# Kernel optimization log

Hardware: AMD Instinct MI355X
Metric: run time of the kernel (lower is better)

The kernel has to match this reference:

```python
import math
import jax, jax.numpy as jnp
import numpy as np

D = 1536      # d_model
H = 12        # n_heads
L = 12        # n_layers
V = 50257     # vocab (hardcoded in module)
P = 1024      # max positions (hardcoded)
B = 1         # batch (must be 1: pos-embed uses arange(len(idx)))
S = 1024      # sequence length


def setup_inputs() -> dict:
    key = jax.random.key(0)
    ks = jax.random.split(key, 10)
    sc = 0.02
    n = lambda k, shape: (jax.random.normal(k, shape, jnp.float32) * sc)
    return {
        "idx": jax.random.randint(ks[0], (B, S), 0, V),
        "mask": jnp.tril(jnp.ones((S, S), jnp.int32)),  # causal mask
        "tok_emb": n(ks[1], (V, D)),
        "pos_emb": n(ks[2], (P, D)),
        "Wqkv": n(ks[3], (L, D, 3 * D)), "bqkv": jnp.zeros((L, 3 * D), jnp.float32),
        "Wo":   n(ks[4], (L, D, D)),     "bo":   jnp.zeros((L, D), jnp.float32),
        "W1":   n(ks[5], (L, D, 4 * D)), "b1":   jnp.zeros((L, 4 * D), jnp.float32),
        "W2":   n(ks[6], (L, 4 * D, D)), "b2":   jnp.zeros((L, D), jnp.float32),
        "ln_g": jnp.ones((D,), jnp.float32), "ln_b": jnp.zeros((D,), jnp.float32),
        "Wout": n(ks[7], (D, D)), "bout": jnp.zeros((D,), jnp.float32),
    }


def _gpt_forward(idx, mask, tok_emb, pos_emb, Wqkv, bqkv, Wo, bo,
                 W1, b1, W2, b2, ln_g, ln_b, Wout, bout):
    b, s = idx.shape
    d = tok_emb.shape[1]
    hd = d // H
    scale = 1.0 / math.sqrt(d)  # note: module divides by sqrt(d_model), not head_dim

    # faithful quirk: position_embedding(arange(len(idx))) -> (B, D), broadcasts since B==1
    x = tok_emb[idx] + pos_emb[:b]  # (B,S,D)

    mask0 = (mask == 0)  # (S,S) -> broadcast over (B,H,S,S)

    def block(x, p):
        wqkv, bqkv_, wo, bo_, w1, b1_, w2, b2_ = p
        qkv = x @ wqkv + bqkv_                       # (B,S,3D)
        q, k, v = jnp.split(qkv, 3, axis=-1)
        q = q.reshape(b, s, H, hd)
        k = k.reshape(b, s, H, hd)
        v = v.reshape(b, s, H, hd)
        scores = jnp.einsum('bqhd,bkhd->bhqk', q, k) * scale
        scores = jnp.where(mask0, -jnp.inf, scores)
        attn = jax.nn.softmax(scores, axis=-2)       # non-standard: softmax over QUERY axis
        o = jnp.einsum('bhqk,bkhd->bqhd', attn, v).reshape(b, s, d)
        x = x + (o @ wo + bo_)                       # attention residual
        x = x + (jax.nn.relu(x @ w1 + b1_) @ w2 + b2_)  # FFN residual (on post-attn x)
        return x, None

    x, _ = jax.lax.scan(block, x, (Wqkv, bqkv, Wo, bo, W1, b1, W2, b2))

    # final LayerNorm (eps=1e-5 like torch default)
    mu = jnp.mean(x, axis=-1, keepdims=True)
    var = jnp.mean(jnp.square(x - mu), axis=-1, keepdims=True)
    xn = (x - mu) * jax.lax.rsqrt(var + 1e-5) * ln_g + ln_b
    return xn @ Wout + bout


def reference(idx, mask, tok_emb, pos_emb, Wqkv, bqkv, Wo, bo,
              W1, b1, W2, b2, ln_g, ln_b, Wout, bout):
    return _gpt_forward(idx, mask, tok_emb, pos_emb, Wqkv, bqkv, Wo, bo,
                        W1, b1, W2, b2, ln_g, ln_b, Wout, bout)
```

## Files before the change

kernel.cpp:

```cpp
#include <hip/hip_runtime.h>
#include <stdint.h>
#include <math.h>

#define D_MODEL 1536
#define NH 12
#define HD 128
#define NL 12
#define SEQ 1024
#define D3 4608
#define D4 6144
#define SCALE 0.025515518153991442f

typedef __attribute__((ext_vector_type(8))) short short8;
typedef __attribute__((ext_vector_type(4))) float floatx4;

__device__ __forceinline__ uint32_t packhi(float a, float b) {
  return (__float_as_uint(a) >> 16) | (__float_as_uint(b) & 0xFFFF0000u);
}
__device__ __forceinline__ float truncf32(float a) {
  return __uint_as_float(__float_as_uint(a) & 0xFFFF0000u);
}
__device__ __forceinline__ void split8v(float4 v0, float4 v1, uint4 &hi, uint4 &lo) {
  hi.x = packhi(v0.x, v0.y); hi.y = packhi(v0.z, v0.w);
  hi.z = packhi(v1.x, v1.y); hi.w = packhi(v1.z, v1.w);
  lo.x = packhi(v0.x - truncf32(v0.x), v0.y - truncf32(v0.y));
  lo.y = packhi(v0.z - truncf32(v0.z), v0.w - truncf32(v0.w));
  lo.z = packhi(v1.x - truncf32(v1.x), v1.y - truncf32(v1.y));
  lo.w = packhi(v1.z - truncf32(v1.z), v1.w - truncf32(v1.w));
}

__device__ __forceinline__ int xcd_chunk_id(int nwg) {
  int orig = blockIdx.x;
  int xcd = orig & 7, pos = orig >> 3;
  int q = nwg >> 3, r = nwg & 7;
  return (xcd < r ? xcd * (q + 1) : r * (q + 1) + (xcd - r) * q) + pos;
}

__global__ __launch_bounds__(256)
void embed_kernel(const int* __restrict__ idx, const float* __restrict__ tok,
                  const float* __restrict__ pos, float* __restrict__ x) {
  int i = blockIdx.x * 256 + threadIdx.x;
  int s = i / D_MODEL;
  int d = i - s * D_MODEL;
  x[i] = tok[(size_t)idx[s] * D_MODEL + d] + pos[d];
}

template<bool RELU, bool RES, int SPLITK, bool TA2>
__global__ __launch_bounds__(256)
void mgemm_kernel(const float* __restrict__ A, const float* __restrict__ Ab,
                  const float* __restrict__ B,
                  const float* __restrict__ bias, const float* __restrict__ res,
                  float* __restrict__ C, int M, int N, int K, int NC, int NR) {
  __shared__ short Ah[128][36], Al[128][36];
  __shared__ short Bh[64][36], Bl[64][36];
  const int tid = threadIdx.x;
  const int lane = tid & 63, wave = tid >> 6;

  const int lid = xcd_chunk_id(NC * NR * SPLITK);
  const int z   = lid / (NC * NR);
  const int rem = lid - z * (NC * NR);
  const int ct  = rem / NR;
  const int rt  = rem - ct * NR;
  const int bm = rt << 7, bn = ct << 6;

  const int wm = (wave >> 1) << 6, wn = (wave & 1) << 5;
  const int fr = lane & 15, fk = (lane >> 4) << 3;
  const int Kc = K / SPLITK;
  const int kbase = (SPLITK > 1) ? z * Kc : 0;

  floatx4 acc[4][2];
#pragma unroll
  for (int i = 0; i < 4; i++)
#pragma unroll
    for (int j = 0; j < 2; j++) acc[i][j] = (floatx4){0.f, 0.f, 0.f, 0.f};

  const int ar = tid >> 1;
  const int ac = (tid & 1) << 4;
  const int bc = tid & 63;
  const int bkq = (tid >> 6) << 3;
  const float* Ag  = A + (size_t)(bm + ar) * K + kbase + ac;
  const float* Ag2 = TA2 ? (Ab + (size_t)(bm + ar) * K + kbase + ac) : nullptr;
  const float* Bg = B + (size_t)(kbase + bkq) * N + bn + bc;

  float a_reg[16];
  float b_reg[8];

  for (int k0 = 0; k0 < Kc; k0 += 32) {
#pragma unroll
    for (int e = 0; e < 4; e++) {
      float4 v = *(const float4*)(Ag + k0 + 4 * e);
      if constexpr (TA2) {
        float4 w = *(const float4*)(Ag2 + k0 + 4 * e);
        v.x += w.x; v.y += w.y; v.z += w.z; v.w += w.w;
      }
      a_reg[4 * e + 0] = v.x; a_reg[4 * e + 1] = v.y;
      a_reg[4 * e + 2] = v.z; a_reg[4 * e + 3] = v.w;
    }
    {
      const float* Bp = Bg + (size_t)k0 * N;
#pragma unroll
      for (int j = 0; j < 8; j++) b_reg[j] = Bp[(size_t)j * N];
    }
    __syncthreads();
#pragma unroll
    for (int e = 0; e < 2; e++) {
      float4 v0 = {a_reg[8 * e + 0], a_reg[8 * e + 1], a_reg[8 * e + 2], a_reg[8 * e + 3]};
      float4 v1 = {a_reg[8 * e + 4], a_reg[8 * e + 5], a_reg[8 * e + 6], a_reg[8 * e + 7]};
      uint4 hi, lo; split8v(v0, v1, hi, lo);
      *(uint4*)&Ah[ar][ac + 8 * e] = hi;
      *(uint4*)&Al[ar][ac + 8 * e] = lo;
    }
    {
      float4 u0 = {b_reg[0], b_reg[1], b_reg[2], b_reg[3]};
      float4 u1 = {b_reg[4], b_reg[5], b_reg[6], b_reg[7]};
      uint4 hi, lo; split8v(u0, u1, hi, lo);
      *(uint4*)&Bh[bc][bkq] = hi;
      *(uint4*)&Bl[bc][bkq] = lo;
    }
    __syncthreads();

    short8 ah[4], al[4], bh[2], bl[2];
#pragma unroll
    for (int i = 0; i < 4; i++) {
      ah[i] = *(const short8*)&Ah[wm + (i << 4) + fr][fk];
      al[i] = *(const short8*)&Al[wm + (i << 4) + fr][fk];
    }
#pragma unroll
    for (int j = 0; j < 2; j++) {
      bh[j] = *(const short8*)&Bh[wn + (j << 4) + fr][fk];
      bl[j] = *(const short8*)&Bl[wn + (j << 4) + fr][fk];
    }
#pragma unroll
    for (int i = 0; i < 4; i++)
#pragma unroll
      for (int j = 0; j < 2; j++) {
        acc[i][j] = __builtin_amdgcn_mfma_f32_16x16x32_bf16(ah[i], bh[j], acc[i][j], 0, 0, 0);
        acc[i][j] = __builtin_amdgcn_mfma_f32_16x16x32_bf16(ah[i], bl[j], acc[i][j], 0, 0, 0);
        acc[i][j] = __builtin_amdgcn_mfma_f32_16x16x32_bf16(al[i], bh[j], acc[i][j], 0, 0, 0);
      }
  }

  const int cr = (lane >> 4) << 2, cc = lane & 15;
  if constexpr (SPLITK > 1) {
    float* Cp = C + (size_t)z * M * N;
#pragma unroll
    for (int j = 0; j < 2; j++) {
      const int col = bn + wn + (j << 4) + cc;
#pragma unroll
      for (int i = 0; i < 4; i++) {
        const int row0 = bm + wm + (i << 4) + cr;
#pragma unroll
        for (int r = 0; r < 4; r++)
          Cp[(size_t)(row0 + r) * N + col] = acc[i][j][r];
      }
    }
  } else {
#pragma unroll
    for (int j = 0; j < 2; j++) {
      const int col = bn + wn + (j << 4) + cc;
      const float bv = bias[col];
#pragma unroll
      for (int i = 0; i < 4; i++) {
        const int row0 = bm + wm + (i << 4) + cr;
#pragma unroll
        for (int r = 0; r < 4; r++) {
          float v = acc[i][j][r] + bv;
          if constexpr (RES) v += res[(size_t)(row0 + r) * N + col];
          if constexpr (RELU) v = fmaxf(v, 0.f);
          C[(size_t)(row0 + r) * N + col] = v;
        }
      }
    }
  }
}

template<int NP, bool HASB, bool RES, bool RELU>
__global__ __launch_bounds__(256)
void combineN_kernel(const float* __restrict__ parts, size_t pstride,
                     const float* __restrict__ bias, const float* __restrict__ res,
                     float* __restrict__ C, int N) {
  const int i = (blockIdx.x * 256 + threadIdx.x) << 2;
  float4 r = *(const float4*)&parts[i];
#pragma unroll
  for (int zz = 1; zz < NP; zz++) {
    float4 a = *(const float4*)&parts[(size_t)zz * pstride + i];
    r.x += a.x; r.y += a.y; r.z += a.z; r.w += a.w;
  }
  if constexpr (HASB) {
    const int col = i % N;
    float4 bv = *(const float4*)&bias[col];
    r.x += bv.x; r.y += bv.y; r.z += bv.z; r.w += bv.w;
  }
  if constexpr (RES) {
    float4 rv = *(const float4*)&res[i];
    r.x += rv.x; r.y += rv.y; r.z += rv.z; r.w += rv.w;
  }
  if constexpr (RELU) {
    r.x = fmaxf(r.x, 0.f); r.y = fmaxf(r.y, 0.f);
    r.z = fmaxf(r.z, 0.f); r.w = fmaxf(r.w, 0.f);
  }
  *(float4*)&C[i] = r;
}

__global__ __launch_bounds__(256)
void scores_kernel(const float* __restrict__ qkv, float* __restrict__ scores,
                   float* __restrict__ pstats) {
  __shared__ short Qh[128][40], Ql[128][40], Kh[128][40], Kl[128][40];
  const int tid = threadIdx.x;
  const int lane = tid & 63, wave = tid >> 6;

  const int lid = xcd_chunk_id(NH * 36);
  const int h = lid / 36;
  int t = lid - h * 36;
  int rr = 0;
  while ((rr + 1) * (rr + 2) / 2 <= t) rr++;
  const int bi = rr << 7;
  const int bj = (t - rr * (rr + 1) / 2) << 7;

  const int wm = (wave >> 1) << 6, wn = (wave & 1) << 6;
  const int fr = lane & 15, fk = (lane >> 4) << 3;
  const float* Q = qkv + h * HD;
  const float* Kp = qkv + D_MODEL + h * HD;

  floatx4 acc[4][4];
#pragma unroll
  for (int i = 0; i < 4; i++)
#pragma unroll
    for (int j = 0; j < 4; j++) acc[i][j] = (floatx4){0.f, 0.f, 0.f, 0.f};

  const int ar = tid >> 1;
  const int ac = (tid & 1) << 4;

  for (int k0 = 0; k0 < HD; k0 += 32) {
    __syncthreads();
    {
      const float* Qp = Q + (size_t)(bi + ar) * D3 + k0 + ac;
#pragma unroll
      for (int e = 0; e < 2; e++) {
        float4 v0 = *(const float4*)(Qp + 8 * e);
        float4 v1 = *(const float4*)(Qp + 8 * e + 4);
        uint4 hi, lo; split8v(v0, v1, hi, lo);
        *(uint4*)&Qh[ar][ac + 8 * e] = hi;
        *(uint4*)&Ql[ar][ac + 8 * e] = lo;
      }
      const float* Kpp = Kp + (size_t)(bj + ar) * D3 + k0 + ac;
#pragma unroll
      for (int e = 0; e < 2; e++) {
        float4 v0 = *(const float4*)(Kpp + 8 * e);
        float4 v1 = *(const float4*)(Kpp + 8 * e + 4);
        uint4 hi, lo; split8v(v0, v1, hi, lo);
        *(uint4*)&Kh[ar][ac + 8 * e] = hi;
        *(uint4*)&Kl[ar][ac + 8 * e] = lo;
      }
    }
    __syncthreads();
    short8 qh[4], ql[4], kh[4], kl[4];
#pragma unroll
    for (int i = 0; i < 4; i++) {
      qh[i] = *(const short8*)&Qh[wm + (i << 4) + fr][fk];
      ql[i] = *(const short8*)&Ql[wm + (i << 4) + fr][fk];
      kh[i] = *(const short8*)&Kh[wn + (i << 4) + fr][fk];
      kl[i] = *(const short8*)&Kl[wn + (i << 4) + fr][fk];
    }
#pragma unroll
    for (int i = 0; i < 4; i++)
#pragma unroll
      for (int j = 0; j < 4; j++) {
        acc[i][j] = __builtin_amdgcn_mfma_f32_16x16x32_bf16(qh[i], kh[j], acc[i][j], 0, 0, 0);
        acc[i][j] = __builtin_amdgcn_mfma_f32_16x16x32_bf16(qh[i], kl[j], acc[i][j], 0, 0, 0);
        acc[i][j] = __builtin_amdgcn_mfma_f32_16x16x32_bf16(ql[i], kh[j], acc[i][j], 0, 0, 0);
        acc[i][j] = __builtin_amdgcn_mfma_f32_16x16x32_bf16(ql[i], kl[j], acc[i][j], 0, 0, 0);
      }
  }

  const int cr = (lane >> 4) << 2, cc = lane & 15;
  float* S = scores + (size_t)h * SEQ * SEQ;
  const int qc = (bi >> 6) + (wave >> 1);
  float* Pm = pstats + (size_t)((h * 16 + qc) * 2 + 0) * 1024;
  float* Pz = pstats + (size_t)((h * 16 + qc) * 2 + 1) * 1024;
#pragma unroll
  for (int j = 0; j < 4; j++) {
    const int col = bj + wn + (j << 4) + cc;
    float vv[16];
    float m = -1e30f;
#pragma unroll
    for (int i = 0; i < 4; i++) {
      const int row0 = bi + wm + (i << 4) + cr;
#pragma unroll
      for (int r = 0; r < 4; r++) {
        float v = (col <= row0 + r) ? acc[i][j][r] * SCALE : -1e30f;
        S[(size_t)(row0 + r) * SEQ + col] = v;
        vv[i * 4 + r] = v;
        m = fmaxf(m, v);
      }
    }
    float zz = 0.f;
#pragma unroll
    for (int t2 = 0; t2 < 16; t2++) zz += __expf(vv[t2] - m);
    if (m == -1e30f) zz = 0.f;
#pragma unroll
    for (int off = 16; off <= 32; off <<= 1) {
      float mo = __shfl_xor(m, off, 64);
      float zo = __shfl_xor(zz, off, 64);
      float mn = fmaxf(m, mo);
      zz = zz * __expf(m - mn) + zo * __expf(mo - mn);
      m = mn;
    }
    if ((lane >> 4) == 0) { Pm[col] = m; Pz[col] = zz; }
  }
}

__global__ __launch_bounds__(256)
void av_kernel(const float* __restrict__ qkv, const float* __restrict__ scores,
               const float* __restrict__ pstats, float* __restrict__ part) {
  __shared__ short Ph[64][40], Pl[64][40], Vh[128][40], Vl[128][40];
  __shared__ float Ms[512], Rs[512];
  const int tid = threadIdx.x;
  const int lane = tid & 63, wave = tid >> 6;

  const int lid = xcd_chunk_id(NH * 32);
  const int h = lid >> 5;
  const int t = lid & 31;
  const int y = t >> 1, z = t & 1;
  const int bm = y << 6;

  const int wm = (wave >> 1) << 5, wn = (wave & 1) << 6;
  const int fr = lane & 15, fk = (lane >> 4) << 3;
  const float* S = scores + (size_t)h * SEQ * SEQ;
  const float* V = qkv + 2 * D_MODEL + h * HD;

  const int kbeg = z * (y + 1) * 32;
  const int kend = (z + 1) * (y + 1) * 32;
  const int ncols = kend - kbeg;

  for (int c0 = tid; c0 < ncols; c0 += 256) {
    const int c = kbeg + c0;
    const int q0 = c >> 6;
    float m = -1e30f;
    for (int qc = q0; qc < 16; qc++)
      m = fmaxf(m, pstats[(size_t)((h * 16 + qc) * 2 + 0) * 1024 + c]);
    float zz = 0.f;
    for (int qc = q0; qc < 16; qc++) {
      float pm = pstats[(size_t)((h * 16 + qc) * 2 + 0) * 1024 + c];
      float pz = pstats[(size_t)((h * 16 + qc) * 2 + 1) * 1024 + c];
      zz += pz * __expf(pm - m);
    }
    Ms[c0] = m;
    Rs[c0] = 1.f / zz;
  }

  floatx4 acc[2][4];
#pragma unroll
  for (int i = 0; i < 2; i++)
#pragma unroll
    for (int j = 0; j < 4; j++) acc[i][j] = (floatx4){0.f, 0.f, 0.f, 0.f};

  const int ar = tid >> 2;
  const int ac = (tid & 3) << 3;
  const int bc = tid & 127;
  const int bkq = (tid >> 7) << 4;

  for (int k0 = kbeg; k0 < kend; k0 += 32) {
    __syncthreads();
    {
      const float* Sp = S + (size_t)(bm + ar) * SEQ + k0 + ac;
      float4 v0 = *(const float4*)(Sp);
      float4 v1 = *(const float4*)(Sp + 4);
      float t8[8] = {v0.x, v0.y, v0.z, v0.w, v1.x, v1.y, v1.z, v1.w};
      float4 p0, p1;
      {
        int kk = k0 - kbeg + ac;
        p0.x = __expf(t8[0] - Ms[kk + 0]) * Rs[kk + 0];
        p0.y = __expf(t8[1] - Ms[kk + 1]) * Rs[kk + 1];
        p0.z = __expf(t8[2] - Ms[kk + 2]) * Rs[kk + 2];
        p0.w = __expf(t8[3] - Ms[kk + 3]) * Rs[kk + 3];
        p1.x = __expf(t8[4] - Ms[kk + 4]) * Rs[kk + 4];
        p1.y = __expf(t8[5] - Ms[kk + 5]) * Rs[kk + 5];
        p1.z = __expf(t8[6] - Ms[kk + 6]) * Rs[kk + 6];
        p1.w = __expf(t8[7] - Ms[kk + 7]) * Rs[kk + 7];
      }
      uint4 hi, lo; split8v(p0, p1, hi, lo);
      *(uint4*)&Ph[ar][ac] = hi;
      *(uint4*)&Pl[ar][ac] = lo;
    }
    {
      const float* Vp = V + (size_t)(k0 + bkq) * D3 + bc;
#pragma unroll
      for (int e = 0; e < 2; e++) {
        float4 u0, u1;
        u0.x = Vp[(size_t)(8 * e + 0) * D3]; u0.y = Vp[(size_t)(8 * e + 1) * D3];
        u0.z = Vp[(size_t)(8 * e + 2) * D3]; u0.w = Vp[(size_t)(8 * e + 3) * D3];
        u1.x = Vp[(size_t)(8 * e + 4) * D3]; u1.y = Vp[(size_t)(8 * e + 5) * D3];
        u1.z = Vp[(size_t)(8 * e + 6) * D3]; u1.w = Vp[(size_t)(8 * e + 7) * D3];
        uint4 hi, lo; split8v(u0, u1, hi, lo);
        *(uint4*)&Vh[bc][bkq + 8 * e] = hi;
        *(uint4*)&Vl[bc][bkq + 8 * e] = lo;
      }
    }
    __syncthreads();
    short8 ph[2], pl[2], vh[4], vl[4];
#pragma unroll
    for (int i = 0; i < 2; i++) {
      ph[i] = *(const short8*)&Ph[wm + (i << 4) + fr][fk];
      pl[i] = *(const short8*)&Pl[wm + (i << 4) + fr][fk];
    }
#pragma unroll
    for (int j = 0; j < 4; j++) {
      vh[j] = *(const short8*)&Vh[wn + (j << 4) + fr][fk];
      vl[j] = *(const short8*)&Vl[wn + (j << 4) + fr][fk];
    }
#pragma unroll
    for (int i = 0; i < 2; i++)
#pragma unroll
      for (int j = 0; j < 4; j++) {
        acc[i][j] = __builtin_amdgcn_mfma_f32_16x16x32_bf16(ph[i], vh[j], acc[i][j], 0, 0, 0);
        acc[i][j] = __builtin_amdgcn_mfma_f32_16x16x32_bf16(ph[i], vl[j], acc[i][j], 0, 0, 0);
        acc[i][j] = __builtin_amdgcn_mfma_f32_16x16x32_bf16(pl[i], vh[j], acc[i][j], 0, 0, 0);
      }
  }

  const int cr = (lane >> 4) << 2, cc = lane & 15;
  float* Cp = part + (size_t)z * SEQ * D_MODEL;
#pragma unroll
  for (int j = 0; j < 4; j++) {
    const int col = h * HD + wn + (j << 4) + cc;
#pragma unroll
    for (int i = 0; i < 2; i++) {
      const int row0 = bm + wm + (i << 4) + cr;
#pragma unroll
      for (int r = 0; r < 4; r++)
        Cp[(size_t)(row0 + r) * D_MODEL + col] = acc[i][j][r];
    }
  }
}

__global__ __launch_bounds__(256)
void ln_kernel(const float* __restrict__ x, const float* __restrict__ g,
               const float* __restrict__ bb, float* __restrict__ y) {
  __shared__ float red[8];
  const int row = blockIdx.x;
  const float* xr = x + (size_t)row * D_MODEL;
  float v[6];
  float s = 0.f, sq = 0.f;
#pragma unroll
  for (int i = 0; i < 6; i++) {
    v[i] = xr[256 * i + threadIdx.x];
    s += v[i];
    sq += v[i] * v[i];
  }
#pragma unroll
  for (int off = 32; off >= 1; off >>= 1) {
    s += __shfl_down(s, off, 64);
    sq += __shfl_down(sq, off, 64);
  }
  const int lane = threadIdx.x & 63, w = threadIdx.x >> 6;
  if (lane == 0) { red[w] = s; red[4 + w] = sq; }
  __syncthreads();
  if (threadIdx.x == 0) {
    red[0] = red[0] + red[1] + red[2] + red[3];
    red[4] = red[4] + red[5] + red[6] + red[7];
  }
  __syncthreads();
  const float mu = red[0] * (1.f / D_MODEL);
  const float var = red[4] * (1.f / D_MODEL) - mu * mu;
  const float rs = rsqrtf(var + 1e-5f);
#pragma unroll
  for (int i = 0; i < 6; i++) {
    int c = 256 * i + threadIdx.x;
    y[(size_t)row * D_MODEL + c] = (v[i] - mu) * rs * g[c] + bb[c];
  }
}

extern "C" void kernel_launch(void* const* d_in, const int* in_sizes, int n_in,
                              void* d_out, int out_size, void* d_ws, size_t ws_size,
                              hipStream_t stream) {
  (void)in_sizes; (void)n_in; (void)out_size; (void)ws_size;
  const int*   idx     = (const int*)d_in[0];
  const float* tok_emb = (const float*)d_in[2];
  const float* pos_emb = (const float*)d_in[3];
  const float* Wqkv    = (const float*)d_in[4];
  const float* bqkv    = (const float*)d_in[5];
  const float* Wo      = (const float*)d_in[6];
  const float* bo      = (const float*)d_in[7];
  const float* W1      = (const float*)d_in[8];
  const float* b1      = (const float*)d_in[9];
  const float* W2      = (const float*)d_in[10];
  const float* b2      = (const float*)d_in[11];
  const float* ln_g    = (const float*)d_in[12];
  const float* ln_b    = (const float*)d_in[13];
  const float* Wout    = (const float*)d_in[14];
  const float* bout    = (const float*)d_in[15];
  float* out = (float*)d_out;

  char* ws = (char*)d_ws;
  float* x      = (float*)(ws);
  float* qkv    = (float*)(ws + 6291456);
  float* pstats = (float*)(ws + 25165824);
  float* part   = (float*)(ws + 26836992);
  float* U      = (float*)(ws + 64585728);
  float* scores = U;
  float* h1     = U;
  float* xn     = U;
  const size_t PN = (size_t)SEQ * D_MODEL;

  embed_kernel<<<6144, 256, 0, stream>>>(idx, tok_emb, pos_emb, x);

  for (int l = 0; l < NL; l++) {
    const float* wqkv = Wqkv + (size_t)l * D_MODEL * D3;
    const float* bq   = bqkv + (size_t)l * D3;
    const float* wo   = Wo   + (size_t)l * D_MODEL * D_MODEL;
    const float* bo_  = bo   + (size_t)l * D_MODEL;
    const float* w1   = W1   + (size_t)l * D_MODEL * D4;
    const float* b1_  = b1   + (size_t)l * D4;
    const float* w2   = W2   + (size_t)l * D4 * D_MODEL;
    const float* b2_  = b2   + (size_t)l * D_MODEL;

    mgemm_kernel<false, false, 1, false><<<576, 256, 0, stream>>>(
        x, nullptr, wqkv, bq, nullptr, qkv, SEQ, D3, D_MODEL, 72, 8);
    scores_kernel<<<432, 256, 0, stream>>>(qkv, scores, pstats);
    av_kernel<<<384, 256, 0, stream>>>(qkv, scores, pstats, part);
    mgemm_kernel<false, false, 4, true><<<768, 256, 0, stream>>>(
        part, part + PN, wo, nullptr, nullptr, part + 2 * PN,
        SEQ, D_MODEL, D_MODEL, 24, 8);
    combineN_kernel<4, true, true, false><<<1536, 256, 0, stream>>>(
        part + 2 * PN, PN, bo_, x, x, D_MODEL);
    mgemm_kernel<true, false, 1, false><<<768, 256, 0, stream>>>(
        x, nullptr, w1, b1_, nullptr, h1, SEQ, D4, D_MODEL, 96, 8);
    mgemm_kernel<false, false, 4, false><<<768, 256, 0, stream>>>(
        h1, nullptr, w2, nullptr, nullptr, part, SEQ, D_MODEL, D4, 24, 8);
    combineN_kernel<4, true, true, false><<<1536, 256, 0, stream>>>(
        part, PN, b2_, x, x, D_MODEL);
  }

  ln_kernel<<<SEQ, 256, 0, stream>>>(x, ln_g, ln_b, xn);
  mgemm_kernel<false, false, 4, false><<<768, 256, 0, stream>>>(
      xn, nullptr, Wout, nullptr, nullptr, part, SEQ, D_MODEL, D_MODEL, 24, 8);
  combineN_kernel<4, true, false, false><<<1536, 256, 0, stream>>>(
      part, PN, bout, nullptr, out, D_MODEL);
}
```

Before: 4.253 ms.

## Split attention AV into four key chunks and split-K the FFN up-projection

The AV kernel now divides each query block's key range into four chunks instead of two, doubling its grid to 768 workgroups. Those four partial outputs are summed inside the Wo GEMM's A-load via a generalized TA template parameter. The W1 GEMM moves to split-K=2 with 1536 workgroups, writing partials to a new buffer; a separate combine kernel then adds the bias and applies ReLU. This raises parallelism in under-filled launches, at the cost of extra partial-buffer traffic, an extra kernel launch per layer and a larger workspace.

```diff
diff --git a/kernel.cpp b/kernel.cpp
--- a/kernel.cpp
+++ b/kernel.cpp
@@ -45,9 +45,9 @@
   x[i] = tok[(size_t)idx[s] * D_MODEL + d] + pos[d];
 }
 
-template<bool RELU, bool RES, int SPLITK, bool TA2>
+template<bool RELU, bool RES, int SPLITK, int TA>
 __global__ __launch_bounds__(256)
-void mgemm_kernel(const float* __restrict__ A, const float* __restrict__ Ab,
+void mgemm_kernel(const float* __restrict__ A, size_t APN,
                   const float* __restrict__ B,
                   const float* __restrict__ bias, const float* __restrict__ res,
                   float* __restrict__ C, int M, int N, int K, int NC, int NR) {
@@ -78,8 +78,7 @@
   const int ac = (tid & 1) << 4;
   const int bc = tid & 63;
   const int bkq = (tid >> 6) << 3;
-  const float* Ag  = A + (size_t)(bm + ar) * K + kbase + ac;
-  const float* Ag2 = TA2 ? (Ab + (size_t)(bm + ar) * K + kbase + ac) : nullptr;
+  const float* Ag = A + (size_t)(bm + ar) * K + kbase + ac;
   const float* Bg = B + (size_t)(kbase + bkq) * N + bn + bc;
 
   float a_reg[16];
@@ -89,9 +88,15 @@
 #pragma unroll
     for (int e = 0; e < 4; e++) {
       float4 v = *(const float4*)(Ag + k0 + 4 * e);
-      if constexpr (TA2) {
-        float4 w = *(const float4*)(Ag2 + k0 + 4 * e);
+      if constexpr (TA >= 2) {
+        float4 w = *(const float4*)(Ag + APN + k0 + 4 * e);
         v.x += w.x; v.y += w.y; v.z += w.z; v.w += w.w;
+      }
+      if constexpr (TA >= 4) {
+        float4 u = *(const float4*)(Ag + 2 * APN + k0 + 4 * e);
+        float4 t = *(const float4*)(Ag + 3 * APN + k0 + 4 * e);
+        v.x += u.x + t.x; v.y += u.y + t.y;
+        v.z += u.z + t.z; v.w += u.w + t.w;
       }
       a_reg[4 * e + 0] = v.x; a_reg[4 * e + 1] = v.y;
       a_reg[4 * e + 2] = v.z; a_reg[4 * e + 3] = v.w;
@@ -318,10 +323,10 @@
   const int tid = threadIdx.x;
   const int lane = tid & 63, wave = tid >> 6;
 
-  const int lid = xcd_chunk_id(NH * 32);
-  const int h = lid >> 5;
-  const int t = lid & 31;
-  const int y = t >> 1, z = t & 1;
+  const int lid = xcd_chunk_id(NH * 64);
+  const int h = lid >> 6;
+  const int t = lid & 63;
+  const int y = t >> 2, z = t & 3;
   const int bm = y << 6;
 
   const int wm = (wave >> 1) << 5, wn = (wave & 1) << 6;
@@ -329,8 +334,9 @@
   const float* S = scores + (size_t)h * SEQ * SEQ;
   const float* V = qkv + 2 * D_MODEL + h * HD;
 
-  const int kbeg = z * (y + 1) * 32;
-  const int kend = (z + 1) * (y + 1) * 32;
+  const int Ssteps = 2 * (y + 1);
+  const int kbeg = ((z * Ssteps) >> 2) * 32;
+  const int kend = (((z + 1) * Ssteps) >> 2) * 32;
   const int ncols = kend - kbeg;
 
   for (int c0 = tid; c0 < ncols; c0 += 256) {
@@ -497,11 +503,13 @@
   float* qkv    = (float*)(ws + 6291456);
   float* pstats = (float*)(ws + 25165824);
   float* part   = (float*)(ws + 26836992);
-  float* U      = (float*)(ws + 64585728);
+  float* U      = (float*)(ws + 77168640);
+  float* partC  = (float*)(ws + 127500288);
   float* scores = U;
   float* h1     = U;
   float* xn     = U;
-  const size_t PN = (size_t)SEQ * D_MODEL;
+  const size_t PN  = (size_t)SEQ * D_MODEL;
+  const size_t PNH = (size_t)SEQ * D4;
 
   embed_kernel<<<6144, 256, 0, stream>>>(idx, tok_emb, pos_emb, x);
 
@@ -515,26 +523,28 @@
     const float* w2   = W2   + (size_t)l * D4 * D_MODEL;
     const float* b2_  = b2   + (size_t)l * D_MODEL;
 
-    mgemm_kernel<false, false, 1, false><<<576, 256, 0, stream>>>(
-        x, nullptr, wqkv, bq, nullptr, qkv, SEQ, D3, D_MODEL, 72, 8);
+    mgemm_kernel<false, false, 1, 1><<<576, 256, 0, stream>>>(
+        x, 0, wqkv, bq, nullptr, qkv, SEQ, D3, D_MODEL, 72, 8);
     scores_kernel<<<432, 256, 0, stream>>>(qkv, scores, pstats);
-    av_kernel<<<384, 256, 0, stream>>>(qkv, scores, pstats, part);
-    mgemm_kernel<false, false, 4, true><<<768, 256, 0, stream>>>(
-        part, part + PN, wo, nullptr, nullptr, part + 2 * PN,
+    av_kernel<<<768, 256, 0, stream>>>(qkv, scores, pstats, part);
+    mgemm_kernel<false, false, 4, 4><<<768, 256, 0, stream>>>(
+        part, PN, wo, nullptr, nullptr, part + 4 * PN,
         SEQ, D_MODEL, D_MODEL, 24, 8);
     combineN_kernel<4, true, true, false><<<1536, 256, 0, stream>>>(
-        part + 2 * PN, PN, bo_, x, x, D_MODEL);
-    mgemm_kernel<true, false, 1, false><<<768, 256, 0, stream>>>(
-        x, nullptr, w1, b1_, nullptr, h1, SEQ, D4, D_MODEL, 96, 8);
-    mgemm_kernel<false, false, 4, false><<<768, 256, 0, stream>>>(
-        h1, nullptr, w2, nullptr, nullptr, part, SEQ, D_MODEL, D4, 24, 8);
+        part + 4 * PN, PN, bo_, x, x, D_MODEL);
+    mgemm_kernel<false, false, 2, 1><<<1536, 256, 0, stream>>>(
+        x, 0, w1, nullptr, nullptr, partC, SEQ, D4, D_MODEL, 96, 8);
+    combineN_kernel<2, true, false, true><<<6144, 256, 0, stream>>>(
+        partC, PNH, b1_, nullptr, h1, D4);
+    mgemm_kernel<false, false, 4, 1><<<768, 256, 0, stream>>>(
+        h1, 0, w2, nullptr, nullptr, part, SEQ, D_MODEL, D4, 24, 8);
     combineN_kernel<4, true, true, false><<<1536, 256, 0, stream>>>(
         part, PN, b2_, x, x, D_MODEL);
   }
 
   ln_kernel<<<SEQ, 256, 0, stream>>>(x, ln_g, ln_b, xn);
-  mgemm_kernel<false, false, 4, false><<<768, 256, 0, stream>>>(
-      xn, nullptr, Wout, nullptr, nullptr, part, SEQ, D_MODEL, D_MODEL, 24, 8);
+  mgemm_kernel<false, false, 4, 1><<<768, 256, 0, stream>>>(
+      xn, 0, Wout, nullptr, nullptr, part, SEQ, D_MODEL, D_MODEL, 24, 8);
   combineN_kernel<4, true, false, false><<<1536, 256, 0, stream>>>(
       part, PN, bout, nullptr, out, D_MODEL);
 }
```

Measured after the change: 4.475 ms. 5.2% more time.
